# Kernel tuning notes

Measured on AMD Instinct MI355X. Metric: run time of the kernel, lower is better.

The kernel has to match this reference:

```python
import jax, jax.numpy as jnp
import numpy as np

O = 64        # group-rep dimension (U_y, U_x are O x O)
C_OUT = 96    # output channel blocks
C_IN = 96     # input channel blocks
SOFTNESS = 0.0


def _build_structure():
    """Build the Schur block structure: 24 2x2 rotation blocks (8 distinct
    angles x 3 copies) + 16 1x1 blocks (+1/-1). sigma_y == sigma_x, so the
    mask marks matching blocks and rows/cols index matched 2x2 sub-blocks."""
    blocks = []
    angles = [0.15 * (k + 1) for k in range(8)]
    for a in angles:
        for _ in range(3):
            blocks.append(('R', round(a, 6)))
    for k in range(16):
        blocks.append(('D', 1.0 if k % 2 == 0 else -1.0))
    dims = [2 if t == 'R' else 1 for t, _ in blocks]
    n = sum(dims)
    assert n == O
    mask = np.zeros((n, n), np.float32)
    rows, cols = [], []
    yc = 0
    for (ti, vi), di in zip(blocks, dims):
        xc = 0
        for (tj, vj), dj in zip(blocks, dims):
            if di == dj and ti == tj and vi == vj:
                mask[yc:yc + di, xc:xc + dj] = 1.0
                if di == 2:
                    rows += [yc, yc, yc + 1, yc + 1]
                    cols += [xc, xc + 1, xc, xc + 1]
            xc += dj
        yc += di
    return mask, np.asarray(rows, np.int32), np.asarray(cols, np.int32)


def setup_inputs() -> dict:
    key = jax.random.key(0)
    k1, k2, k3 = jax.random.split(key, 3)
    W = jax.random.normal(k1, (C_OUT * O, C_IN * O), jnp.float32)
    # Orthogonal Schur bases via QR of Gaussian matrices
    U_y = jnp.linalg.qr(jax.random.normal(k2, (O, O), jnp.float32))[0]
    U_x = jnp.linalg.qr(jax.random.normal(k3, (O, O), jnp.float32))[0]
    mask_np, rows_np, cols_np = _build_structure()
    return {
        'W': W,
        'U_y': U_y,
        'U_x': U_x,
        'mask': jnp.asarray(mask_np),
        'block_rows': jnp.asarray(rows_np),
        'block_cols': jnp.asarray(cols_np),
    }


def reference(W, U_y, U_x, mask, block_rows, block_cols):
    o = U_y.shape[0]
    i = U_x.shape[0]
    c_out = W.shape[-2] // o
    c_in = W.shape[-1] // i
    # _to_blocks: (c_out*o, c_in*i) -> (c_out, c_in, o, i)
    Wb = W.reshape(c_out, o, c_in, i).transpose(0, 2, 1, 3)
    # W' = U_y.T @ W @ U_x, then apply sparsity mask
    Wp = jnp.einsum('po,bcpq,qk->bcok', U_y, Wb, U_x) * mask
    # Gather matched 2x2 sub-blocks: (c_out, c_in, num_blocks, 2, 2)
    nb = block_rows.shape[0] // 4
    g = Wp[..., block_rows, block_cols].reshape(c_out, c_in, nb, 2, 2)
    alpha = (g[..., 0, 0] + g[..., 1, 1]) * 0.5
    beta = (g[..., 0, 1] - g[..., 1, 0]) * 0.5
    hard = jnp.stack([jnp.stack([alpha, beta], axis=-1),
                      jnp.stack([-beta, alpha], axis=-1)], axis=-2)
    soft = SOFTNESS * g + (1.0 - SOFTNESS) * hard
    # Scatter symmetrized blocks back (index pairs are unique)
    Wp = Wp.at[..., block_rows, block_cols].set(soft.reshape(c_out, c_in, -1))
    # W_out = U_y @ W'_proj @ U_x.T
    out_b = jnp.einsum('op,bcpq,kq->bcok', U_y, Wp, U_x)
    # _from_blocks: (c_out, c_in, o, i) -> (c_out*o, c_in*i)
    return out_b.transpose(0, 2, 1, 3).reshape(c_out * o, c_in * i)
```

## Files before the change

### kernel.cpp

```cpp
#include <hip/hip_runtime.h>


#define NB  96
#define NW  6144
#define LDP 72

typedef _Float16 f16;
typedef _Float16 half8 __attribute__((ext_vector_type(8)));
typedef _Float16 half4 __attribute__((ext_vector_type(4)));
typedef float    f32x4 __attribute__((ext_vector_type(4)));

__device__ __forceinline__ half8 ld8(const f16* p) {
    return *reinterpret_cast<const half8*>(p);
}
__device__ __forceinline__ float xor1(float x) {
    return __builtin_bit_cast(float,
        __builtin_amdgcn_mov_dpp(__builtin_bit_cast(int, x), 0xB1, 0xF, 0xF, true));
}

__global__ void prep_u(const float* __restrict__ Uy, const float* __restrict__ Ux,
                       f16* __restrict__ Upack) {
    int idx = blockIdx.x * 256 + threadIdx.x;
    int r = idx >> 6, c = idx & 63;
    int p = ((r >> 4) * 2 + (c >> 5)) * 512 + (((c & 31) >> 3) * 16 + (r & 15)) * 8 + (c & 7);
    Upack[0 * 4096 + p] = (f16)Ux[c * 64 + r];
    Upack[1 * 4096 + p] = (f16)Uy[c * 64 + r];
    Upack[2 * 4096 + p] = (f16)Ux[r * 64 + c];
    Upack[3 * 4096 + p] = (f16)Uy[r * 64 + c];
}

__global__ __launch_bounds__(256, 4)
void schur_fused(const float* __restrict__ W,
                 const f16* __restrict__ Upack,
                 float* __restrict__ out) {
    __shared__ f16 lds[4][64 * LDP];

    const int t  = threadIdx.x;
    const int w  = t >> 6;
    const int l  = t & 63;
    const int lr = l & 15;
    const int lg = l >> 4;

    const int blk = blockIdx.x * 4 + w;
    const int bo  = blk / NB;
    const int bc  = blk % NB;

    f16* buf = lds[w];

    const f16* UxTi = Upack;
    const f16* UyTi = Upack + 4096;
    const f16* Uxi  = Upack + 8192;
    const f16* Uyi  = Upack + 12288;

    {
        const int cr = l >> 4;
        const int cc = l & 15;
        const float* srcb = W + (size_t)(bo * 64 + cr) * NW + bc * 64 + cc * 4;
        f16* dstb = buf + cr * LDP + cc * 4;
        float4 vc[4], vn[4];
#pragma unroll
        for (int q = 0; q < 4; ++q)
            vn[q] = *reinterpret_cast<const float4*>(srcb + (size_t)(q * 16) * NW);
#pragma unroll
        for (int grp = 0; grp < 4; ++grp) {
#pragma unroll
            for (int q = 0; q < 4; ++q) vc[q] = vn[q];
            if (grp < 3) {
#pragma unroll
                for (int q = 0; q < 4; ++q)
                    vn[q] = *reinterpret_cast<const float4*>(
                        srcb + (size_t)((grp + 1) * 4 + q * 16) * NW);
            }
#pragma unroll
            for (int q = 0; q < 4; ++q) {
                half4 h = { (f16)vc[q].x, (f16)vc[q].y, (f16)vc[q].z, (f16)vc[q].w };
                *reinterpret_cast<half4*>(dstb + (q * 4 + grp) * 4 * LDP) = h;
            }
        }
    }

    f32x4 acc[4][4];
    half8 b[4][2];

    auto ldbI = [&](const f16* img) {
#pragma unroll
        for (int ct = 0; ct < 4; ++ct) {
            b[ct][0] = ld8(img + (ct * 2 + 0) * 512 + l * 8);
            b[ct][1] = ld8(img + (ct * 2 + 1) * 512 + l * 8);
        }
    };
    auto mmAL = [&]() {
#pragma unroll
        for (int rt = 0; rt < 4; ++rt) {
            const f16* ar = buf + (rt * 16 + lr) * LDP + lg * 8;
            half8 a0 = ld8(ar), a1 = ld8(ar + 32);
#pragma unroll
            for (int ct = 0; ct < 4; ++ct) {
                f32x4 d = {0.f, 0.f, 0.f, 0.f};
                d = __builtin_amdgcn_mfma_f32_16x16x32_f16(a0, b[ct][0], d, 0, 0, 0);
                d = __builtin_amdgcn_mfma_f32_16x16x32_f16(a1, b[ct][1], d, 0, 0, 0);
                acc[rt][ct] = d;
            }
        }
    };
    auto wrT = [&]() {
#pragma unroll
        for (int rt = 0; rt < 4; ++rt)
#pragma unroll
            for (int ct = 0; ct < 4; ++ct) {
                f32x4 v = acc[rt][ct];
                half4 h = { (f16)v[0], (f16)v[1], (f16)v[2], (f16)v[3] };
                *reinterpret_cast<half4*>(buf + (ct * 16 + lr) * LDP + rt * 16 + lg * 4) = h;
            }
    };

    ldbI(UxTi); mmAL(); wrT();
    ldbI(UyTi); mmAL();

#pragma unroll
    for (int rt = 0; rt < 4; ++rt) {
        const int kbase = rt * 16 + lg * 4;
#pragma unroll
        for (int ct = 0; ct < 4; ++ct) {
            const int o = ct * 16 + lr;
            const float s = (o & 1) ? -1.f : 1.f;
            const bool oeven = ((o & 1) == 0);
#pragma unroll
            for (int p = 0; p < 2; ++p) {
                const int k0 = kbase + 2 * p;
                float x0 = acc[rt][ct][2 * p];
                float x1 = acc[rt][ct][2 * p + 1];
                float t0 = xor1(x0);
                float t1 = xor1(x1);
                const bool Ract = (o < 48) && (k0 < 48) &&
                                  ((o * 43 >> 8) == (k0 * 43 >> 8));
                const bool Dact = (o >= 48) && (k0 >= 48);
                float r0v = 0.5f * (x0 + s * t1);
                float r1v = 0.5f * (x1 - s * t0);
                float d0 = oeven ? x0 : 0.f;
                float d1 = oeven ? 0.f : x1;
                acc[rt][ct][2 * p]     = Ract ? r0v : (Dact ? d0 : 0.f);
                acc[rt][ct][2 * p + 1] = Ract ? r1v : (Dact ? d1 : 0.f);
            }
        }
    }

    wrT();
    ldbI(Uxi); mmAL(); wrT();
    ldbI(Uyi); mmAL();

    {
#pragma unroll
        for (int ct = 0; ct < 4; ++ct) {
            float* rowp = out + (size_t)(bo * 64 + ct * 16 + lr) * NW + bc * 64 + lg * 4;
#pragma unroll
            for (int rt = 0; rt < 4; ++rt)
                *reinterpret_cast<f32x4*>(rowp + rt * 16) = acc[rt][ct];
        }
    }
}

extern "C" void kernel_launch(void* const* d_in, const int* in_sizes, int n_in,
                              void* d_out, int out_size, void* d_ws, size_t ws_size,
                              hipStream_t stream) {
    const float* W  = (const float*)d_in[0];
    const float* Uy = (const float*)d_in[1];
    const float* Ux = (const float*)d_in[2];

    f16*   Upack = (f16*)d_ws;
    float* o     = (float*)d_out;

    prep_u<<<dim3(16), 256, 0, stream>>>(Uy, Ux, Upack);
    schur_fused<<<dim3(NB * NB / 4), 256, 0, stream>>>(W, Upack, o);
}
```

Baseline: 81.36 us.

## Stream MFMA row tiles through LDS with swizzled layout to cut registers

```diff
diff --git a/kernel.cpp b/kernel.cpp
--- a/kernel.cpp
+++ b/kernel.cpp
@@ -3,7 +3,6 @@
 
 #define NB  96
 #define NW  6144
-#define LDP 72
 
 typedef _Float16 f16;
 typedef _Float16 half8 __attribute__((ext_vector_type(8)));
@@ -12,6 +11,9 @@
 
 __device__ __forceinline__ half8 ld8(const f16* p) {
     return *reinterpret_cast<const half8*>(p);
+}
+__device__ __forceinline__ float4 ldf4(const float* p) {
+    return *reinterpret_cast<const float4*>(p);
 }
 __device__ __forceinline__ float xor1(float x) {
     return __builtin_bit_cast(float,
@@ -29,11 +31,11 @@
     Upack[3 * 4096 + p] = (f16)Uy[r * 64 + c];
 }
 
-__global__ __launch_bounds__(256, 4)
+__global__ __launch_bounds__(256, 5)
 void schur_fused(const float* __restrict__ W,
                  const f16* __restrict__ Upack,
                  float* __restrict__ out) {
-    __shared__ f16 lds[4][64 * LDP];
+    __shared__ f16 lds[4][4096];
 
     const int t  = threadIdx.x;
     const int w  = t >> 6;
@@ -45,7 +47,7 @@
     const int bo  = blk / NB;
     const int bc  = blk % NB;
 
-    f16* buf = lds[w];
+    char* bufb = (char*)lds[w];
 
     const f16* UxTi = Upack;
     const f16* UyTi = Upack + 4096;
@@ -53,14 +55,13 @@
     const f16* Uyi  = Upack + 12288;
 
     {
-        const int cr = l >> 4;
-        const int cc = l & 15;
+        const int cr = lg;
+        const int cc = lr;
         const float* srcb = W + (size_t)(bo * 64 + cr) * NW + bc * 64 + cc * 4;
-        f16* dstb = buf + cr * LDP + cc * 4;
         float4 vc[4], vn[4];
 #pragma unroll
         for (int q = 0; q < 4; ++q)
-            vn[q] = *reinterpret_cast<const float4*>(srcb + (size_t)(q * 16) * NW);
+            vn[q] = ldf4(srcb + (size_t)(q * 16) * NW);
 #pragma unroll
         for (int grp = 0; grp < 4; ++grp) {
 #pragma unroll
@@ -68,18 +69,20 @@
             if (grp < 3) {
 #pragma unroll
                 for (int q = 0; q < 4; ++q)
-                    vn[q] = *reinterpret_cast<const float4*>(
-                        srcb + (size_t)((grp + 1) * 4 + q * 16) * NW);
+                    vn[q] = ldf4(srcb + (size_t)((grp + 1) * 4 + q * 16) * NW);
             }
 #pragma unroll
             for (int q = 0; q < 4; ++q) {
-                half4 h = { (f16)vc[q].x, (f16)vc[q].y, (f16)vc[q].z, (f16)vc[q].w };
-                *reinterpret_cast<half4*>(dstb + (q * 4 + grp) * 4 * LDP) = h;
+                float4 v = vc[q];
+                half4 h = { (f16)v.x, (f16)v.y, (f16)v.z, (f16)v.w };
+                const int row = cr + 4 * grp + 16 * q;
+                *reinterpret_cast<half4*>(bufb + row * 128 +
+                                          ((cc * 8) ^ ((row & 7) << 4))) = h;
             }
         }
     }
 
-    f32x4 acc[4][4];
+    f32x4 acc[4];
     half8 b[4][2];
 
     auto ldbI = [&](const f16* img) {
@@ -89,36 +92,41 @@
             b[ct][1] = ld8(img + (ct * 2 + 1) * 512 + l * 8);
         }
     };
-    auto mmAL = [&]() {
-#pragma unroll
-        for (int rt = 0; rt < 4; ++rt) {
-            const f16* ar = buf + (rt * 16 + lr) * LDP + lg * 8;
-            half8 a0 = ld8(ar), a1 = ld8(ar + 32);
-#pragma unroll
-            for (int ct = 0; ct < 4; ++ct) {
-                f32x4 d = {0.f, 0.f, 0.f, 0.f};
-                d = __builtin_amdgcn_mfma_f32_16x16x32_f16(a0, b[ct][0], d, 0, 0, 0);
-                d = __builtin_amdgcn_mfma_f32_16x16x32_f16(a1, b[ct][1], d, 0, 0, 0);
-                acc[rt][ct] = d;
-            }
+    auto mfma8p = [&](half8 a0, half8 a1) {
+#pragma unroll
+        for (int ct = 0; ct < 4; ++ct) {
+            f32x4 d = {0.f, 0.f, 0.f, 0.f};
+            d = __builtin_amdgcn_mfma_f32_16x16x32_f16(a0, b[ct][0], d, 0, 0, 0);
+            d = __builtin_amdgcn_mfma_f32_16x16x32_f16(a1, b[ct][1], d, 0, 0, 0);
+            acc[ct] = d;
         }
     };
-    auto wrT = [&]() {
-#pragma unroll
-        for (int rt = 0; rt < 4; ++rt)
-#pragma unroll
-            for (int ct = 0; ct < 4; ++ct) {
-                f32x4 v = acc[rt][ct];
-                half4 h = { (f16)v[0], (f16)v[1], (f16)v[2], (f16)v[3] };
-                *reinterpret_cast<half4*>(buf + (ct * 16 + lr) * LDP + rt * 16 + lg * 4) = h;
-            }
-    };
-
-    ldbI(UxTi); mmAL(); wrT();
-    ldbI(UyTi); mmAL();
-
-#pragma unroll
-    for (int rt = 0; rt < 4; ++rt) {
+
+    ldbI(UxTi);
+#pragma unroll
+    for (int rt = 0; rt < 4; ++rt) {
+        const int row = rt * 16 + lr;
+        const int swz = (lr & 7) << 4;
+        half8 a0 = ld8((const f16*)(bufb + row * 128 + ((lg * 16) ^ swz)));
+        half8 a1 = ld8((const f16*)(bufb + row * 128 + ((lg * 16 + 64) ^ swz)));
+        mfma8p(a0, a1);
+#pragma unroll
+        for (int ct = 0; ct < 4; ++ct) {
+            f32x4 v = acc[ct];
+            half4 h = { (f16)v[0], (f16)v[1], (f16)v[2], (f16)v[3] };
+            *reinterpret_cast<half4*>(bufb + rt * 2048 + (ct * 16 + lr) * 32 + lg * 8) = h;
+        }
+    }
+
+    ldbI(UyTi);
+#pragma unroll
+    for (int rt = 0; rt < 4; ++rt) {
+        half8 a0 = ld8((const f16*)(bufb + (lg >> 1) * 2048 +
+                                    (rt * 16 + lr) * 32 + (lg & 1) * 16));
+        half8 a1 = ld8((const f16*)(bufb + (2 + (lg >> 1)) * 2048 +
+                                    (rt * 16 + lr) * 32 + (lg & 1) * 16));
+        mfma8p(a0, a1);
+
         const int kbase = rt * 16 + lg * 4;
 #pragma unroll
         for (int ct = 0; ct < 4; ++ct) {
@@ -128,8 +136,8 @@
 #pragma unroll
             for (int p = 0; p < 2; ++p) {
                 const int k0 = kbase + 2 * p;
-                float x0 = acc[rt][ct][2 * p];
-                float x1 = acc[rt][ct][2 * p + 1];
+                float x0 = acc[ct][2 * p];
+                float x1 = acc[ct][2 * p + 1];
                 float t0 = xor1(x0);
                 float t1 = xor1(x1);
                 const bool Ract = (o < 48) && (k0 < 48) &&
@@ -139,23 +147,54 @@
                 float r1v = 0.5f * (x1 - s * t0);
                 float d0 = oeven ? x0 : 0.f;
                 float d1 = oeven ? 0.f : x1;
-                acc[rt][ct][2 * p]     = Ract ? r0v : (Dact ? d0 : 0.f);
-                acc[rt][ct][2 * p + 1] = Ract ? r1v : (Dact ? d1 : 0.f);
+                acc[ct][2 * p]     = Ract ? r0v : (Dact ? d0 : 0.f);
+                acc[ct][2 * p + 1] = Ract ? r1v : (Dact ? d1 : 0.f);
             }
         }
-    }
-
-    wrT();
-    ldbI(Uxi); mmAL(); wrT();
-    ldbI(Uyi); mmAL();
-
-    {
-#pragma unroll
-        for (int ct = 0; ct < 4; ++ct) {
-            float* rowp = out + (size_t)(bo * 64 + ct * 16 + lr) * NW + bc * 64 + lg * 4;
-#pragma unroll
-            for (int rt = 0; rt < 4; ++rt)
-                *reinterpret_cast<f32x4*>(rowp + rt * 16) = acc[rt][ct];
+
+#pragma unroll
+        for (int ct = 0; ct < 4; ++ct) {
+            f32x4 v = acc[ct];
+            half4 h = { (f16)v[0], (f16)v[1], (f16)v[2], (f16)v[3] };
+            *reinterpret_cast<half4*>(bufb + ct * 2048 + rt * 512 + lr * 32 + lg * 8) = h;
+        }
+    }
+
+    ldbI(Uxi);
+#pragma unroll
+    for (int rt = 0; rt < 4; ++rt) {
+        half8 a0 = ld8((const f16*)(bufb + rt * 2048 + (lg >> 1) * 512 +
+                                    lr * 32 + (lg & 1) * 16));
+        half8 a1 = ld8((const f16*)(bufb + rt * 2048 + (2 + (lg >> 1)) * 512 +
+                                    lr * 32 + (lg & 1) * 16));
+        mfma8p(a0, a1);
+#pragma unroll
+        for (int ct = 0; ct < 4; ++ct) {
+            f32x4 v = acc[ct];
+            half4 h = { (f16)v[0], (f16)v[1], (f16)v[2], (f16)v[3] };
+            *reinterpret_cast<half4*>(bufb + rt * 2048 + (ct * 16 + lr) * 32 + lg * 8) = h;
+        }
+    }
+
+#pragma unroll
+    for (int ct = 0; ct < 4; ++ct) {
+        b[ct][0] = ld8((const f16*)(bufb + (lg >> 1) * 2048 +
+                                    (ct * 16 + lr) * 32 + (lg & 1) * 16));
+        b[ct][1] = ld8((const f16*)(bufb + (2 + (lg >> 1)) * 2048 +
+                                    (ct * 16 + lr) * 32 + (lg & 1) * 16));
+    }
+#pragma unroll
+    for (int rt = 0; rt < 4; ++rt) {
+        half8 a0 = ld8(Uyi + (rt * 2 + 0) * 512 + l * 8);
+        half8 a1 = ld8(Uyi + (rt * 2 + 1) * 512 + l * 8);
+        mfma8p(a0, a1);
+        float* ob = out + (size_t)(bo * 64 + rt * 16 + lg * 4) * NW + bc * 64 + lr;
+#pragma unroll
+        for (int i = 0; i < 4; ++i) {
+            float* rp = ob + (size_t)i * NW;
+#pragma unroll
+            for (int ct = 0; ct < 4; ++ct)
+                rp[ct * 16] = acc[ct][i];
         }
     }
 }
```

Measured after the change: 133.6 us. 1.64x slower.
